# Optimization experiments

Measured on AMD Instinct MI355X. Metric: run time of the kernel, lower is better.

The kernel has to match this reference:

```python
import jax, jax.numpy as jnp
import numpy as np

N = 8  # nodes per sample (hardcoded in preprocess)
NEG_SLOPE = 0.2
BIG_NEG = -1e30


def _mlp3(x, w1, b1, w2, b2, w3, b3):
    h = jax.nn.relu(x @ w1 + b1)
    h = jax.nn.relu(h @ w2 + b2)
    return h @ w3 + b3


def _gabriel(p):
    # p: [B,N,3] (vis_latent). Returns symmetric boolean adjacency [B,N,N]
    # (no self loops) and pairwise distances [B,N,N].
    mid = (p[:, :, None, :] + p[:, None, :, :]) * 0.5          # [B,N,N,3]
    r2 = jnp.sum((p[:, :, None, :] - mid) ** 2, axis=-1)       # [B,N,N]
    # d2[b,i,j,k] = ||p[b,k] - mid[b,i,j]||^2
    d2 = jnp.sum((p[:, None, None, :, :] - mid[:, :, :, None, :]) ** 2, axis=-1)  # [B,N,N,N]
    eye = jnp.eye(N, dtype=bool)
    kmask = (~eye[:, None, :]) & (~eye[None, :, :])            # [N,N,N] k != i, k != j
    viol = jnp.any(kmask[None] & (d2 < r2[..., None]), axis=-1)
    adj = (~viol) & (~eye)[None]                               # [B,N,N]
    dist = jnp.sqrt(jnp.sum((p[:, :, None, :] - p[:, None, :, :]) ** 2, axis=-1) + 1e-30)
    return adj, dist


def _gatv2(x, mask, eattr, wl, bl, wr, br, we, att, bias):
    # Dense masked GATv2 (PyG semantics, heads=1).
    # x: [B,N,F]; mask: [B,N,N] bool (row i = target, col j = source);
    # eattr: [B,N,N,1] edge feature.
    xl = x @ wl + bl                                            # source transform [B,N,C]
    xr = x @ wr + br                                            # target transform [B,N,C]
    ee = eattr @ we                                             # [B,N,N,C]
    h = xr[:, :, None, :] + xl[:, None, :, :] + ee              # [B,N,N,C]
    h = jnp.where(h >= 0, h, NEG_SLOPE * h)                     # leaky_relu
    e = jnp.einsum('bijc,c->bij', h, att)
    e = jnp.where(mask, e, BIG_NEG)
    alpha = jax.nn.softmax(e, axis=-1) * mask                   # rows always contain self loop
    return jnp.einsum('bij,bjc->bic', alpha, xl) + bias


def _forward(x, enc_w1, enc_b1, enc_w2, enc_b2, enc_w3, enc_b3,
             g1_wl, g1_bl, g1_wr, g1_br, g1_we, g1_att, g1_bias,
             g2_wl, g2_bl, g2_wr, g2_br, g2_we, g2_att, g2_bias,
             skip_w, skip_b, dec_w1, dec_b1, dec_w2, dec_b2, dec_w3, dec_b3):
    B = x.shape[0]
    # preprocess: [agent_type=0, index, value]
    idx = jnp.broadcast_to(jnp.arange(N, dtype=x.dtype), (B, N))
    xp = jnp.stack([jnp.zeros_like(x), idx, x], axis=-1)        # [B,N,3]

    latent = _mlp3(xp, enc_w1, enc_b1, enc_w2, enc_b2, enc_w3, enc_b3)  # [B,N,3]
    vis = latent - jnp.mean(latent, axis=1, keepdims=True)
    std = jnp.std(vis, axis=1, ddof=1) + 1e-8                   # torch.std is unbiased
    vis = vis / std[:, None, :]

    adj, dist = _gabriel(vis)                                   # [B,N,N] bool / float
    eye = jnp.eye(N, dtype=bool)[None]
    mask = adj | eye                                            # add self loops
    n_edges = jnp.sum(adj, axis=(1, 2)).astype(x.dtype)
    mean_attr = jnp.sum(dist * adj, axis=(1, 2)) / jnp.maximum(n_edges, 1.0)
    eattr = jnp.where(eye, mean_attr[:, None, None], dist)[..., None]  # [B,N,N,1]

    h1 = jax.nn.relu(_gatv2(latent, mask, eattr, g1_wl, g1_bl, g1_wr, g1_br, g1_we, g1_att, g1_bias))
    h2 = _gatv2(h1, mask, eattr, g2_wl, g2_bl, g2_wr, g2_br, g2_we, g2_att, g2_bias)
    combined = h2 + latent @ skip_w + skip_b
    rec = _mlp3(combined, dec_w1, dec_b1, dec_w2, dec_b2, dec_w3, dec_b3)
    return xp, rec, vis, adj


def setup_inputs() -> dict:
    key = jax.random.key(0)
    ks = iter(jax.random.split(key, 32))
    B, H, L, F = 16384, 64, 3, 3

    def rn(shape, scale):
        return (jax.random.normal(next(ks), shape, dtype=jnp.float32) * scale)

    inp = {
        'x': jax.random.normal(next(ks), (B, N), dtype=jnp.float32),
        'enc_w1': rn((F, H), (1.0 / F) ** 0.5), 'enc_b1': jnp.zeros((H,), jnp.float32),
        'enc_w2': rn((H, H), (1.0 / H) ** 0.5), 'enc_b2': jnp.zeros((H,), jnp.float32),
        'enc_w3': rn((H, L), (1.0 / H) ** 0.5), 'enc_b3': jnp.zeros((L,), jnp.float32),
        'g1_wl': rn((L, H), (1.0 / L) ** 0.5), 'g1_bl': jnp.zeros((H,), jnp.float32),
        'g1_wr': rn((L, H), (1.0 / L) ** 0.5), 'g1_br': jnp.zeros((H,), jnp.float32),
        'g1_we': rn((1, H), 1.0), 'g1_att': rn((H,), (1.0 / H) ** 0.5),
        'g1_bias': jnp.zeros((H,), jnp.float32),
        'g2_wl': rn((H, L), (1.0 / H) ** 0.5), 'g2_bl': jnp.zeros((L,), jnp.float32),
        'g2_wr': rn((H, L), (1.0 / H) ** 0.5), 'g2_br': jnp.zeros((L,), jnp.float32),
        'g2_we': rn((1, L), 1.0), 'g2_att': rn((L,), (1.0 / L) ** 0.5),
        'g2_bias': jnp.zeros((L,), jnp.float32),
        'skip_w': rn((L, L), (1.0 / L) ** 0.5), 'skip_b': jnp.zeros((L,), jnp.float32),
        'dec_w1': rn((L, H), (1.0 / L) ** 0.5), 'dec_b1': jnp.zeros((H,), jnp.float32),
        'dec_w2': rn((H, H), (1.0 / H) ** 0.5), 'dec_b2': jnp.zeros((H,), jnp.float32),
        'dec_w3': rn((H, F), (1.0 / H) ** 0.5), 'dec_b3': jnp.zeros((F,), jnp.float32),
    }
    return inp


def reference(x, enc_w1, enc_b1, enc_w2, enc_b2, enc_w3, enc_b3,
              g1_wl, g1_bl, g1_wr, g1_br, g1_we, g1_att, g1_bias,
              g2_wl, g2_bl, g2_wr, g2_br, g2_we, g2_att, g2_bias,
              skip_w, skip_b, dec_w1, dec_b1, dec_w2, dec_b2, dec_w3, dec_b3):
    return _forward(x, enc_w1, enc_b1, enc_w2, enc_b2, enc_w3, enc_b3,
                    g1_wl, g1_bl, g1_wr, g1_br, g1_we, g1_att, g1_bias,
                    g2_wl, g2_bl, g2_wr, g2_br, g2_we, g2_att, g2_bias,
                    skip_w, skip_b, dec_w1, dec_b1, dec_w2, dec_b2, dec_w3, dec_b3)
```

## Files before the change

kernel.cpp:

```cpp
#include <hip/hip_runtime.h>
#include <math.h>


struct alignas(16) WaveScratch {
  union Big {
    double d[8][68];
    float  f[2][8][68];
  } big;
  float  alphaS[64];
  float  latSf[24];
  float  xl2S[24];
  float  xr2S[24];
  float  combS[24];
  double latSd[24];
  double visSd[24];
};

__global__ __launch_bounds__(256)
void gae_fused(const float* __restrict__ x,
               const float* __restrict__ enc_w1, const float* __restrict__ enc_b1,
               const float* __restrict__ enc_w2, const float* __restrict__ enc_b2,
               const float* __restrict__ enc_w3, const float* __restrict__ enc_b3,
               const float* __restrict__ g1_wl, const float* __restrict__ g1_bl,
               const float* __restrict__ g1_wr, const float* __restrict__ g1_br,
               const float* __restrict__ g1_we, const float* __restrict__ g1_att,
               const float* __restrict__ g1_bias,
               const float* __restrict__ g2_wl, const float* __restrict__ g2_bl,
               const float* __restrict__ g2_wr, const float* __restrict__ g2_br,
               const float* __restrict__ g2_we, const float* __restrict__ g2_att,
               const float* __restrict__ g2_bias,
               const float* __restrict__ skip_w, const float* __restrict__ skip_b,
               const float* __restrict__ dec_w1, const float* __restrict__ dec_b1,
               const float* __restrict__ dec_w2, const float* __restrict__ dec_b2,
               const float* __restrict__ dec_w3, const float* __restrict__ dec_b3,
               float* __restrict__ out, int B)
{
  __shared__ WaveScratch ws4[4];
  __shared__ __align__(16) float s_w3e[192];
  __shared__ __align__(16) float s_w3d[192];
  __shared__ __align__(16) float s_g2wl[192];
  __shared__ __align__(16) float s_g2wr[192];
  __shared__ __align__(16) float s_we1[64];
  __shared__ __align__(16) float s_att1[64];
  __shared__ float s_skw[9], s_skb[3], s_b3e[3], s_b3d[3];
  __shared__ float s_g2bl[3], s_g2br[3], s_g2we[3], s_g2att[3], s_g2bias[3];

  const int tid  = threadIdx.x;
  const int wid  = tid >> 6;
  const int lane = tid & 63;

  if (tid < 192) { s_w3e[tid] = enc_w3[tid]; s_w3d[tid] = dec_w3[tid];
                   s_g2wl[tid] = g2_wl[tid]; s_g2wr[tid] = g2_wr[tid]; }
  if (tid < 64)  { s_we1[tid] = g1_we[tid];  s_att1[tid] = g1_att[tid]; }
  if (tid < 9)   s_skw[tid] = skip_w[tid];
  if (tid < 3)   { s_skb[tid] = skip_b[tid]; s_b3e[tid] = enc_b3[tid]; s_b3d[tid] = dec_b3[tid];
                   s_g2bl[tid] = g2_bl[tid]; s_g2br[tid] = g2_br[tid]; s_g2we[tid] = g2_we[tid];
                   s_g2att[tid] = g2_att[tid]; s_g2bias[tid] = g2_bias[tid]; }

  const int s = blockIdx.x * 4 + wid;
  const bool active = (s < B);
  const int sc = active ? s : 0;
  WaveScratch& W = ws4[wid];

  const double ew1n = (double)enc_w1[64 + lane];
  const double ew1x = (double)enc_w1[128 + lane];
  const double eb1d = (double)enc_b1[lane];
  const double eb2d = (double)enc_b2[lane];
  const float wl0 = g1_wl[lane], wl1 = g1_wl[64 + lane], wl2 = g1_wl[128 + lane], blc = g1_bl[lane];
  const float wr0 = g1_wr[lane], wr1 = g1_wr[64 + lane], wr2 = g1_wr[128 + lane], brc = g1_br[lane];
  const float g1bias_c = g1_bias[lane];
  const float dwc0 = dec_w1[lane], dwc1 = dec_w1[64 + lane], dwc2 = dec_w1[128 + lane];
  const float db1c = dec_b1[lane], db2c = dec_b2[lane];

  __syncthreads();

  const float* xb = x + (size_t)sc * 8;
  if (active && lane < 24) {
    const int r = lane, n = r / 3, l = r - n * 3;
    float v = (l == 0) ? 0.0f : ((l == 1) ? (float)n : xb[n]);
    out[(size_t)s * 24 + r] = v;
  }
  #pragma unroll
  for (int n = 0; n < 8; ++n) {
    double v = (double)n * ew1n + (double)xb[n] * ew1x + eb1d;
    W.big.d[n][lane] = v > 0.0 ? v : 0.0;
  }
  __syncthreads();

  double acc2[8];
  #pragma unroll
  for (int n = 0; n < 8; ++n) acc2[n] = eb2d;
  #pragma unroll
  for (int ch = 0; ch < 4; ++ch) {
    double wcd[16];
    #pragma unroll
    for (int t = 0; t < 16; ++t) wcd[t] = (double)enc_w2[(ch * 16 + t) * 64 + lane];
    #pragma unroll
    for (int t2 = 0; t2 < 8; ++t2) {
      #pragma unroll
      for (int n = 0; n < 8; ++n) {
        const double2 hv = *(const double2*)&W.big.d[n][ch * 16 + t2 * 2];
        acc2[n] = fma(hv.x, wcd[t2 * 2], acc2[n]);
        acc2[n] = fma(hv.y, wcd[t2 * 2 + 1], acc2[n]);
      }
    }
  }
  __syncthreads();
  #pragma unroll
  for (int n = 0; n < 8; ++n) W.big.d[n][lane] = acc2[n] > 0.0 ? acc2[n] : 0.0;
  __syncthreads();

  if (lane < 24) {
    const int r = lane, n = r / 3, l = r - n * 3;
    double a = (double)s_b3e[l];
    #pragma unroll 8
    for (int k = 0; k < 64; ++k) a = fma(W.big.d[n][k], (double)s_w3e[k * 3 + l], a);
    W.latSd[r] = a;
    W.latSf[r] = (float)a;
  }
  __syncthreads();

  if (lane < 24) {
    const int r = lane, n = r / 3, l = r - n * 3; (void)n;
    double s1 = 0.0;
    #pragma unroll
    for (int q = 0; q < 8; ++q) s1 += W.latSd[q * 3 + l];
    const double m = s1 * 0.125;
    double s2 = 0.0;
    #pragma unroll
    for (int q = 0; q < 8; ++q) s2 += (W.latSd[q * 3 + l] - m);
    const double m2 = s2 * 0.125;
    double s3 = 0.0;
    #pragma unroll
    for (int q = 0; q < 8; ++q) { double dv = W.latSd[q * 3 + l] - m - m2; s3 += dv * dv; }
    const double stdv = sqrt(s3 / 7.0) + 1e-8;
    const double visv = (W.latSd[r] - m) / stdv;
    W.visSd[r] = visv;
    if (active) out[(size_t)B * 48 + (size_t)s * 24 + r] = (float)visv;
  }
  __syncthreads();

  const int gi = lane >> 3, gj = lane & 7;
  const double pi0 = W.visSd[gi * 3], pi1 = W.visSd[gi * 3 + 1], pi2 = W.visSd[gi * 3 + 2];
  const double pj0 = W.visSd[gj * 3], pj1 = W.visSd[gj * 3 + 1], pj2 = W.visSd[gj * 3 + 2];
  const double mid0 = (pi0 + pj0) * 0.5, mid1 = (pi1 + pj1) * 0.5, mid2 = (pi2 + pj2) * 0.5;
  const double dr0 = pi0 - mid0, dr1 = pi1 - mid1, dr2 = pi2 - mid2;
  const double r2 = dr0 * dr0 + dr1 * dr1 + dr2 * dr2;
  bool viol = false;
  #pragma unroll
  for (int k = 0; k < 8; ++k) {
    const double a0 = W.visSd[k * 3] - mid0;
    const double a1 = W.visSd[k * 3 + 1] - mid1;
    const double a2 = W.visSd[k * 3 + 2] - mid2;
    const double d2 = a0 * a0 + a1 * a1 + a2 * a2;
    viol = viol || ((k != gi) && (k != gj) && (d2 < r2));
  }
  const double dd0 = pi0 - pj0, dd1 = pi1 - pj1, dd2 = pi2 - pj2;
  const double distd = sqrt(dd0 * dd0 + dd1 * dd1 + dd2 * dd2 + 1e-30);
  const bool adjb  = (!viol) && (gi != gj);
  const bool maskb = adjb || (gi == gj);
  const float adjf = adjb ? 1.0f : 0.0f;
  if (active) out[(size_t)B * 72 + (size_t)s * 64 + lane] = adjf;
  const float distf = (float)distd;
  float ne = adjf, sd = adjb ? distf : 0.0f;
  #pragma unroll
  for (int d = 1; d < 64; d <<= 1) { ne += __shfl_xor(ne, d); sd += __shfl_xor(sd, d); }
  const float mean_attr = sd / fmaxf(ne, 1.0f);
  const float eat = (gi == gj) ? mean_attr : distf;

  float xlr[8], xrr[8];
  #pragma unroll
  for (int n = 0; n < 8; ++n) {
    const float a0 = W.latSf[n * 3], a1 = W.latSf[n * 3 + 1], a2 = W.latSf[n * 3 + 2];
    xlr[n] = fmaf(a2, wl2, fmaf(a1, wl1, fmaf(a0, wl0, blc)));
    xrr[n] = fmaf(a2, wr2, fmaf(a1, wr1, fmaf(a0, wr0, brc)));
    W.big.f[0][n][lane] = xlr[n];
    W.big.f[1][n][lane] = xrr[n];
  }
  __syncthreads();

  float ev = 0.0f;
  #pragma unroll
  for (int c4 = 0; c4 < 16; ++c4) {
    const float4 xlv = *(const float4*)&W.big.f[0][gj][c4 * 4];
    const float4 xrv = *(const float4*)&W.big.f[1][gi][c4 * 4];
    const float4 wev = *(const float4*)&s_we1[c4 * 4];
    const float4 atv = *(const float4*)&s_att1[c4 * 4];
    float h;
    h = fmaf(eat, wev.x, xrv.x + xlv.x); ev = fmaf(fmaxf(h, 0.f) + 0.2f * fminf(h, 0.f), atv.x, ev);
    h = fmaf(eat, wev.y, xrv.y + xlv.y); ev = fmaf(fmaxf(h, 0.f) + 0.2f * fminf(h, 0.f), atv.y, ev);
    h = fmaf(eat, wev.z, xrv.z + xlv.z); ev = fmaf(fmaxf(h, 0.f) + 0.2f * fminf(h, 0.f), atv.z, ev);
    h = fmaf(eat, wev.w, xrv.w + xlv.w); ev = fmaf(fmaxf(h, 0.f) + 0.2f * fminf(h, 0.f), atv.w, ev);
  }
  {
    float em = maskb ? ev : -1e30f;
    float mx = em;
    mx = fmaxf(mx, __shfl_xor(mx, 1)); mx = fmaxf(mx, __shfl_xor(mx, 2)); mx = fmaxf(mx, __shfl_xor(mx, 4));
    float p = __expf(em - mx);
    float ssum = p;
    ssum += __shfl_xor(ssum, 1); ssum += __shfl_xor(ssum, 2); ssum += __shfl_xor(ssum, 4);
    W.alphaS[lane] = (p / ssum) * (maskb ? 1.0f : 0.0f);
  }
  __syncthreads();

  float hg[8];
  #pragma unroll
  for (int i = 0; i < 8; ++i) {
    const float4 q0 = *(const float4*)&W.alphaS[i * 8];
    const float4 q1 = *(const float4*)&W.alphaS[i * 8 + 4];
    float a = g1bias_c;
    a = fmaf(q0.x, xlr[0], a); a = fmaf(q0.y, xlr[1], a);
    a = fmaf(q0.z, xlr[2], a); a = fmaf(q0.w, xlr[3], a);
    a = fmaf(q1.x, xlr[4], a); a = fmaf(q1.y, xlr[5], a);
    a = fmaf(q1.z, xlr[6], a); a = fmaf(q1.w, xlr[7], a);
    hg[i] = fmaxf(a, 0.0f);
  }
  __syncthreads();
  #pragma unroll
  for (int i = 0; i < 8; ++i) W.big.f[0][i][lane] = hg[i];
  __syncthreads();

  if (lane < 48) {
    const int g = lane / 24, r = lane - g * 24, n = r / 3, l = r - n * 3;
    const float* wsel = g ? s_g2wr : s_g2wl;
    float a = g ? s_g2br[l] : s_g2bl[l];
    #pragma unroll 8
    for (int k = 0; k < 64; ++k) a = fmaf(W.big.f[0][n][k], wsel[k * 3 + l], a);
    if (g) W.xr2S[r] = a; else W.xl2S[r] = a;
  }
  __syncthreads();

  float e2 = 0.0f;
  #pragma unroll
  for (int l = 0; l < 3; ++l) {
    const float hh = fmaf(eat, s_g2we[l], W.xr2S[gi * 3 + l] + W.xl2S[gj * 3 + l]);
    e2 = fmaf(fmaxf(hh, 0.f) + 0.2f * fminf(hh, 0.f), s_g2att[l], e2);
  }
  {
    float em = maskb ? e2 : -1e30f;
    float mx = em;
    mx = fmaxf(mx, __shfl_xor(mx, 1)); mx = fmaxf(mx, __shfl_xor(mx, 2)); mx = fmaxf(mx, __shfl_xor(mx, 4));
    float p = __expf(em - mx);
    float ssum = p;
    ssum += __shfl_xor(ssum, 1); ssum += __shfl_xor(ssum, 2); ssum += __shfl_xor(ssum, 4);
    W.alphaS[lane] = (p / ssum) * (maskb ? 1.0f : 0.0f);
  }
  __syncthreads();

  if (lane < 24) {
    const int r = lane, n = r / 3, l = r - n * 3;
    float a = s_g2bias[l];
    #pragma unroll
    for (int j = 0; j < 8; ++j) a = fmaf(W.alphaS[n * 8 + j], W.xl2S[j * 3 + l], a);
    const float cb = a + W.latSf[n * 3] * s_skw[l] + W.latSf[n * 3 + 1] * s_skw[3 + l]
                       + W.latSf[n * 3 + 2] * s_skw[6 + l] + s_skb[l];
    W.combS[r] = cb;
  }
  __syncthreads();

  #pragma unroll
  for (int n = 0; n < 8; ++n) {
    const float c0 = W.combS[n * 3], c1 = W.combS[n * 3 + 1], c2 = W.combS[n * 3 + 2];
    const float d1 = fmaf(c2, dwc2, fmaf(c1, dwc1, fmaf(c0, dwc0, db1c)));
    W.big.f[0][n][lane] = fmaxf(d1, 0.0f);
  }
  __syncthreads();

  float accf[8];
  #pragma unroll
  for (int n = 0; n < 8; ++n) accf[n] = db2c;
  #pragma unroll
  for (int ch = 0; ch < 2; ++ch) {
    float wc[32];
    #pragma unroll
    for (int t = 0; t < 32; ++t) wc[t] = dec_w2[(ch * 32 + t) * 64 + lane];
    #pragma unroll
    for (int t4 = 0; t4 < 8; ++t4) {
      #pragma unroll
      for (int n = 0; n < 8; ++n) {
        const float4 hv = *(const float4*)&W.big.f[0][n][ch * 32 + t4 * 4];
        accf[n] = fmaf(hv.x, wc[t4 * 4], accf[n]);
        accf[n] = fmaf(hv.y, wc[t4 * 4 + 1], accf[n]);
        accf[n] = fmaf(hv.z, wc[t4 * 4 + 2], accf[n]);
        accf[n] = fmaf(hv.w, wc[t4 * 4 + 3], accf[n]);
      }
    }
  }
  #pragma unroll
  for (int n = 0; n < 8; ++n) W.big.f[1][n][lane] = fmaxf(accf[n], 0.0f);
  __syncthreads();

  if (active && lane < 24) {
    const int r = lane, n = r / 3, l = r - n * 3;
    float a = s_b3d[l];
    #pragma unroll 8
    for (int k = 0; k < 64; ++k) a = fmaf(W.big.f[1][n][k], s_w3d[k * 3 + l], a);
    out[(size_t)B * 24 + (size_t)s * 24 + r] = a;
  }
}

extern "C" void kernel_launch(void* const* d_in, const int* in_sizes, int n_in,
                              void* d_out, int out_size, void* d_ws, size_t ws_size,
                              hipStream_t stream) {
  const int B = in_sizes[0] / 8;
  const float* x       = (const float*)d_in[0];
  const float* enc_w1  = (const float*)d_in[1];
  const float* enc_b1  = (const float*)d_in[2];
  const float* enc_w2  = (const float*)d_in[3];
  const float* enc_b2  = (const float*)d_in[4];
  const float* enc_w3  = (const float*)d_in[5];
  const float* enc_b3  = (const float*)d_in[6];
  const float* g1_wl   = (const float*)d_in[7];
  const float* g1_bl   = (const float*)d_in[8];
  const float* g1_wr   = (const float*)d_in[9];
  const float* g1_br   = (const float*)d_in[10];
  const float* g1_we   = (const float*)d_in[11];
  const float* g1_att  = (const float*)d_in[12];
  const float* g1_bias = (const float*)d_in[13];
  const float* g2_wl   = (const float*)d_in[14];
  const float* g2_bl   = (const float*)d_in[15];
  const float* g2_wr   = (const float*)d_in[16];
  const float* g2_br   = (const float*)d_in[17];
  const float* g2_we   = (const float*)d_in[18];
  const float* g2_att  = (const float*)d_in[19];
  const float* g2_bias = (const float*)d_in[20];
  const float* skip_w  = (const float*)d_in[21];
  const float* skip_b  = (const float*)d_in[22];
  const float* dec_w1  = (const float*)d_in[23];
  const float* dec_b1  = (const float*)d_in[24];
  const float* dec_w2  = (const float*)d_in[25];
  const float* dec_b2  = (const float*)d_in[26];
  const float* dec_w3  = (const float*)d_in[27];
  const float* dec_b3  = (const float*)d_in[28];
  float* out = (float*)d_out;

  const int nblk = (B + 3) / 4;
  gae_fused<<<nblk, 256, 0, stream>>>(x,
      enc_w1, enc_b1, enc_w2, enc_b2, enc_w3, enc_b3,
      g1_wl, g1_bl, g1_wr, g1_br, g1_we, g1_att, g1_bias,
      g2_wl, g2_bl, g2_wr, g2_br, g2_we, g2_att, g2_bias,
      skip_w, skip_b, dec_w1, dec_b1, dec_w2, dec_b2, dec_w3, dec_b3,
      out, B);
}
```

Before: 105.7 us.

## Replace block barriers with per-wave LDS waits and split 64-wide reductions across lanes

Each wave owns its own scratch area, so the block-wide __syncthreads calls become s_waitcnt lgkmcnt(0) fences that only wait on the wave's own LDS operations. This removes cross-wave barrier stalls in a 256-thread block. The encoder and decoder final 64-term dot products are also split across both half-waves and combined with a shuffle, which halves the serial loop length. The risk is correctness: the shared weight arrays loaded before the first kept barrier are still protected, but per-wave ordering now depends on lockstep wave execution and the compiler not reordering LDS accesses.

```diff
diff --git a/kernel.cpp b/kernel.cpp
--- a/kernel.cpp
+++ b/kernel.cpp
@@ -1,6 +1,8 @@
 #include <hip/hip_runtime.h>
 #include <math.h>
 
+
+#define WFENCE() asm volatile("s_waitcnt lgkmcnt(0)" ::: "memory")
 
 struct alignas(16) WaveScratch {
   union Big {
@@ -85,7 +87,7 @@
     double v = (double)n * ew1n + (double)xb[n] * ew1x + eb1d;
     W.big.d[n][lane] = v > 0.0 ? v : 0.0;
   }
-  __syncthreads();
+  WFENCE();
 
   double acc2[8];
   #pragma unroll
@@ -105,23 +107,32 @@
       }
     }
   }
-  __syncthreads();
+  WFENCE();
   #pragma unroll
   for (int n = 0; n < 8; ++n) W.big.d[n][lane] = acc2[n] > 0.0 ? acc2[n] : 0.0;
-  __syncthreads();
+  WFENCE();
+
+  {
+    const int r24 = lane & 31, g = lane >> 5;
+    double a = 0.0;
+    if (r24 < 24) {
+      const int n = r24 / 3, l = r24 - n * 3;
+      a = g ? 0.0 : (double)s_b3e[l];
+      const int k0 = g * 32;
+      #pragma unroll 8
+      for (int k = k0; k < k0 + 32; ++k) a = fma(W.big.d[n][k], (double)s_w3e[k * 3 + l], a);
+    }
+    const double b = __shfl_xor(a, 32);
+    if (lane < 24) {
+      const double tot = a + b;
+      W.latSd[lane] = tot;
+      W.latSf[lane] = (float)tot;
+    }
+  }
+  WFENCE();
 
   if (lane < 24) {
-    const int r = lane, n = r / 3, l = r - n * 3;
-    double a = (double)s_b3e[l];
-    #pragma unroll 8
-    for (int k = 0; k < 64; ++k) a = fma(W.big.d[n][k], (double)s_w3e[k * 3 + l], a);
-    W.latSd[r] = a;
-    W.latSf[r] = (float)a;
-  }
-  __syncthreads();
-
-  if (lane < 24) {
-    const int r = lane, n = r / 3, l = r - n * 3; (void)n;
+    const int r = lane, l = r % 3;
     double s1 = 0.0;
     #pragma unroll
     for (int q = 0; q < 8; ++q) s1 += W.latSd[q * 3 + l];
@@ -138,7 +149,7 @@
     W.visSd[r] = visv;
     if (active) out[(size_t)B * 48 + (size_t)s * 24 + r] = (float)visv;
   }
-  __syncthreads();
+  WFENCE();
 
   const int gi = lane >> 3, gj = lane & 7;
   const double pi0 = W.visSd[gi * 3], pi1 = W.visSd[gi * 3 + 1], pi2 = W.visSd[gi * 3 + 2];
@@ -177,7 +188,7 @@
     W.big.f[0][n][lane] = xlr[n];
     W.big.f[1][n][lane] = xrr[n];
   }
-  __syncthreads();
+  WFENCE();
 
   float ev = 0.0f;
   #pragma unroll
@@ -201,7 +212,7 @@
     ssum += __shfl_xor(ssum, 1); ssum += __shfl_xor(ssum, 2); ssum += __shfl_xor(ssum, 4);
     W.alphaS[lane] = (p / ssum) * (maskb ? 1.0f : 0.0f);
   }
-  __syncthreads();
+  WFENCE();
 
   float hg[8];
   #pragma unroll
@@ -215,10 +226,10 @@
     a = fmaf(q1.z, xlr[6], a); a = fmaf(q1.w, xlr[7], a);
     hg[i] = fmaxf(a, 0.0f);
   }
-  __syncthreads();
+  WFENCE();
   #pragma unroll
   for (int i = 0; i < 8; ++i) W.big.f[0][i][lane] = hg[i];
-  __syncthreads();
+  WFENCE();
 
   if (lane < 48) {
     const int g = lane / 24, r = lane - g * 24, n = r / 3, l = r - n * 3;
@@ -228,7 +239,7 @@
     for (int k = 0; k < 64; ++k) a = fmaf(W.big.f[0][n][k], wsel[k * 3 + l], a);
     if (g) W.xr2S[r] = a; else W.xl2S[r] = a;
   }
-  __syncthreads();
+  WFENCE();
 
   float e2 = 0.0f;
   #pragma unroll
@@ -245,7 +256,7 @@
     ssum += __shfl_xor(ssum, 1); ssum += __shfl_xor(ssum, 2); ssum += __shfl_xor(ssum, 4);
     W.alphaS[lane] = (p / ssum) * (maskb ? 1.0f : 0.0f);
   }
-  __syncthreads();
+  WFENCE();
 
   if (lane < 24) {
     const int r = lane, n = r / 3, l = r - n * 3;
@@ -256,7 +267,7 @@
                        + W.latSf[n * 3 + 2] * s_skw[6 + l] + s_skb[l];
     W.combS[r] = cb;
   }
-  __syncthreads();
+  WFENCE();
 
   #pragma unroll
   for (int n = 0; n < 8; ++n) {
@@ -264,7 +275,7 @@
     const float d1 = fmaf(c2, dwc2, fmaf(c1, dwc1, fmaf(c0, dwc0, db1c)));
     W.big.f[0][n][lane] = fmaxf(d1, 0.0f);
   }
-  __syncthreads();
+  WFENCE();
 
   float accf[8];
   #pragma unroll
@@ -286,16 +297,25 @@
       }
     }
   }
+  WFENCE();
   #pragma unroll
   for (int n = 0; n < 8; ++n) W.big.f[1][n][lane] = fmaxf(accf[n], 0.0f);
-  __syncthreads();
-
-  if (active && lane < 24) {
-    const int r = lane, n = r / 3, l = r - n * 3;
-    float a = s_b3d[l];
-    #pragma unroll 8
-    for (int k = 0; k < 64; ++k) a = fmaf(W.big.f[1][n][k], s_w3d[k * 3 + l], a);
-    out[(size_t)B * 24 + (size_t)s * 24 + r] = a;
+  WFENCE();
+
+  {
+    const int r24 = lane & 31, g = lane >> 5;
+    float a = 0.0f;
+    if (r24 < 24) {
+      const int n = r24 / 3, l = r24 - n * 3;
+      a = g ? 0.0f : s_b3d[l];
+      const int k0 = g * 32;
+      #pragma unroll 8
+      for (int k = k0; k < k0 + 32; ++k) a = fmaf(W.big.f[1][n][k], s_w3d[k * 3 + l], a);
+    }
+    const float b = __shfl_xor(a, 32);
+    if (active && lane < 24) {
+      out[(size_t)B * 24 + (size_t)s * 24 + lane] = a + b;
+    }
   }
 }
 
```

Measured after the change: 95.40 us. 9.7% less time.
